# Performance work log

Measured on AMD Instinct MI355X. Metric: run time of the kernel, lower is better.

Reference implementation:

```python
import jax, jax.numpy as jnp
import numpy as np

# Module hyperparams (from init_kwargs)
MAX_DISP = 4
DILA = 1
P = 2 * MAX_DISP // DILA + 1  # patch_size = 9 -> 81 output channels


def setup_inputs() -> dict:
    key = jax.random.key(0)
    k0, k1 = jax.random.split(key)
    B, C, H, W = 4, 256, 96, 160
    return {
        "fmap0": jax.random.normal(k0, (B, C, H, W), dtype=jnp.float32),
        "fmap1": jax.random.normal(k1, (B, C, H, W), dtype=jnp.float32),
    }


def reference(fmap0, fmap1):
    """SpatialCorrelationSampler(kernel_size=1, patch_size=P, stride=1,
    padding=0, dilation=1, dilation_patch=DILA), reshaped to (B, P*P, H, W).

    corr[b, p, y, x] = sum_c fmap0[b,c,y,x] * fmap1[b,c,y+dy_p,x+dx_p]
    with (dy,dx) in {-MAX_DISP..MAX_DISP step DILA}; out-of-bounds -> 0
    (no channel normalization, matching the CUDA sampler).
    """
    B, C, H, W = fmap0.shape
    D = MAX_DISP
    # Zero-pad fmap1 so every displacement is a static-size slice.
    padded = jnp.pad(fmap1, ((0, 0), (0, 0), (D, D), (D, D)))
    oy, ox = jnp.meshgrid(jnp.arange(P) * DILA, jnp.arange(P) * DILA, indexing="ij")
    offs = jnp.stack([oy.ravel(), ox.ravel()], axis=1)  # (P*P, 2)

    def one_disp(off):
        # window of fmap1 shifted by (off - D): (B, C, H, W)
        win = jax.lax.dynamic_slice(padded, (0, 0, off[0], off[1]), (B, C, H, W))
        return jnp.einsum("bchw,bchw->bhw", fmap0, win)

    corr = jax.lax.map(one_disp, offs)  # (P*P, B, H, W), avoids P^2*C blowup
    return jnp.transpose(corr, (1, 0, 2, 3))  # (B, P*P, H, W)
```

## Files before the change

kernel.cpp:

```cpp
#include <hip/hip_runtime.h>


#define Bn 4
#define Cn 256
#define Hn 96
#define Wn 160
#define HWn (Hn * Wn)
#define NP 81
#define TY 16
#define TX 16
#define CCH 4
#define NSTAGE (Cn / CCH)
#define WROWS (TY + 8)
#define WCOLS (TX + 8)
#define SEGS (WCOLS / 4)
#define LROW 28
#define F1C (WROWS * LROW)
#define NT 576
#define F1CHUNK4 (CCH * HWn / 4)

__global__ __launch_bounds__(NT, 2) void corr_kernel(const float* __restrict__ f0,
                                                     const float* __restrict__ f1,
                                                     float* __restrict__ out) {
    __shared__ __align__(16) float lds[2 * CCH * F1C];

    const int tid  = threadIdx.x;
    const int wave = tid >> 6;
    const int lane = tid & 63;
    const int r    = lane >> 2;
    const int g    = lane & 3;

    const int tile = blockIdx.x;
    const int b    = tile / 60;
    const int rem  = tile % 60;
    const int ty   = rem / 10;
    const int tx   = rem - ty * 10;
    const int y0   = ty * TY;
    const int x0   = tx * TX;

    const int scc  = tid / (WROWS * SEGS);
    const int srm  = tid - scc * (WROWS * SEGS);
    const int srr  = srm / SEGS;
    const int sseg = srm - srr * SEGS;
    const int sgy  = y0 - 4 + srr;
    const int sgx  = x0 - 4 + sseg * 4;
    const bool sval = (sgy >= 0) && (sgy < Hn) && (sgx >= 0) && (sgx < Wn);
    const int slidx = (scc * F1C + srr * LROW + sseg * 4) >> 2;
    const int sgidx = sval ? ((((b * Cn + scc) * Hn + sgy) * Wn + sgx) >> 2) : 0;

    const float4* __restrict__ f1v = (const float4*)f1;
    float4* lv = (float4*)lds;

    float4 p1 = make_float4(0.f, 0.f, 0.f, 0.f);
    if (sval) p1 = f1v[sgidx];

    const float* f0s = f0 + ((b * Cn) * Hn + y0 + r) * Wn + x0 + g * 4;
    float4 p0[CCH];
#pragma unroll
    for (int cc = 0; cc < CCH; ++cc) p0[cc] = *(const float4*)(f0s + cc * HWn);

    float acc[9][4];
#pragma unroll
    for (int i = 0; i < 9; ++i)
#pragma unroll
        for (int j = 0; j < 4; ++j) acc[i][j] = 0.f;

    for (int s = 0; s < NSTAGE; ++s) {
        lv[(s & 1) * (CCH * F1C / 4) + slidx] = p1;
        __syncthreads();

        const int ns = (s + 1 < NSTAGE) ? s + 1 : NSTAGE - 1;
        float4 n1 = make_float4(0.f, 0.f, 0.f, 0.f);
        if (sval) n1 = f1v[sgidx + ns * F1CHUNK4];
        float4 n0[CCH];
#pragma unroll
        for (int cc = 0; cc < CCH; ++cc)
            n0[cc] = *(const float4*)(f0s + (ns * CCH + cc) * HWn);

        const float* base = &lds[(s & 1) * (CCH * F1C) + (r + wave) * LROW + g * 4];
#pragma unroll
        for (int cc = 0; cc < CCH; ++cc) {
            const float* wr = base + cc * F1C;
            float4 w0 = *(const float4*)(wr);
            float4 w1 = *(const float4*)(wr + 4);
            float4 w2 = *(const float4*)(wr + 8);
            float av[4]  = {p0[cc].x, p0[cc].y, p0[cc].z, p0[cc].w};
            float wv[12] = {w0.x, w0.y, w0.z, w0.w, w1.x, w1.y, w1.z, w1.w,
                            w2.x, w2.y, w2.z, w2.w};
#pragma unroll
            for (int dx = 0; dx < 9; ++dx)
#pragma unroll
                for (int rx = 0; rx < 4; ++rx)
                    acc[dx][rx] = fmaf(av[rx], wv[rx + dx], acc[dx][rx]);
        }

        p1 = n1;
#pragma unroll
        for (int cc = 0; cc < CCH; ++cc) p0[cc] = n0[cc];
    }

    const int orow = ((b * NP + wave * 9) * Hn + y0 + r) * Wn + x0 + g * 4;
#pragma unroll
    for (int dx = 0; dx < 9; ++dx)
        *(float4*)(out + orow + dx * HWn) =
            make_float4(acc[dx][0], acc[dx][1], acc[dx][2], acc[dx][3]);
}

extern "C" void kernel_launch(void* const* d_in, const int* in_sizes, int n_in,
                              void* d_out, int out_size, void* d_ws, size_t ws_size,
                              hipStream_t stream) {
    const float* f0 = (const float*)d_in[0];
    const float* f1 = (const float*)d_in[1];
    float* out = (float*)d_out;
    corr_kernel<<<dim3(240), NT, 0, stream>>>(f0, f1, out);
}
```

Baseline: 195.7 us.

## Double channels per pipeline stage and remap blocks for XCD-local L2 reuse

Each stage now covers 8 channels instead of 4, so the loop runs half as many iterations and half as many block barriers. Each thread stages two fmap1 float4s per stage, and each thread keeps 8 float4s of fmap0 current plus 8 prefetched. Block indices are also remapped so that blocks sharing the same XCD (blk&7) work on the same batch and neighbouring row tiles, with the aim of improving L2 locality for the overlapping halo. The main risk is register pressure: the doubled fmap0 buffers under launch_bounds(576,2) could cause spills or lower occupancy.

```diff
diff --git a/kernel.cpp b/kernel.cpp
--- a/kernel.cpp
+++ b/kernel.cpp
@@ -9,20 +9,20 @@
 #define NP 81
 #define TY 16
 #define TX 16
-#define CCH 4
+#define CCH 8
 #define NSTAGE (Cn / CCH)
 #define WROWS (TY + 8)
-#define WCOLS (TX + 8)
-#define SEGS (WCOLS / 4)
+#define SEGS 6
 #define LROW 28
 #define F1C (WROWS * LROW)
+#define BUF (CCH * F1C)
 #define NT 576
-#define F1CHUNK4 (CCH * HWn / 4)
+#define F1STG (CCH * HWn / 4)
 
 __global__ __launch_bounds__(NT, 2) void corr_kernel(const float* __restrict__ f0,
                                                      const float* __restrict__ f1,
                                                      float* __restrict__ out) {
-    __shared__ __align__(16) float lds[2 * CCH * F1C];
+    __shared__ __align__(16) float lds[2 * BUF];
 
     const int tid  = threadIdx.x;
     const int wave = tid >> 6;
@@ -30,13 +30,14 @@
     const int r    = lane >> 2;
     const int g    = lane & 3;
 
-    const int tile = blockIdx.x;
-    const int b    = tile / 60;
-    const int rem  = tile % 60;
-    const int ty   = rem / 10;
-    const int tx   = rem - ty * 10;
-    const int y0   = ty * TY;
-    const int x0   = tx * TX;
+    const int blk = blockIdx.x;
+    const int xcd = blk & 7;
+    const int it  = blk >> 3;
+    const int b   = xcd >> 1;
+    const int ty  = (xcd & 1) * 3 + it / 10;
+    const int tx  = it % 10;
+    const int y0  = ty * TY;
+    const int x0  = tx * TX;
 
     const int scc  = tid / (WROWS * SEGS);
     const int srm  = tid - scc * (WROWS * SEGS);
@@ -51,8 +52,8 @@
     const float4* __restrict__ f1v = (const float4*)f1;
     float4* lv = (float4*)lds;
 
-    float4 p1 = make_float4(0.f, 0.f, 0.f, 0.f);
-    if (sval) p1 = f1v[sgidx];
+    float4 p1a = make_float4(0.f, 0.f, 0.f, 0.f), p1b = p1a;
+    if (sval) { p1a = f1v[sgidx]; p1b = f1v[sgidx + HWn]; }
 
     const float* f0s = f0 + ((b * Cn) * Hn + y0 + r) * Wn + x0 + g * 4;
     float4 p0[CCH];
@@ -66,18 +67,20 @@
         for (int j = 0; j < 4; ++j) acc[i][j] = 0.f;
 
     for (int s = 0; s < NSTAGE; ++s) {
-        lv[(s & 1) * (CCH * F1C / 4) + slidx] = p1;
+        float4* buf = lv + (s & 1) * (BUF / 4);
+        buf[slidx]       = p1a;
+        buf[slidx + F1C] = p1b;
         __syncthreads();
 
         const int ns = (s + 1 < NSTAGE) ? s + 1 : NSTAGE - 1;
-        float4 n1 = make_float4(0.f, 0.f, 0.f, 0.f);
-        if (sval) n1 = f1v[sgidx + ns * F1CHUNK4];
+        float4 n1a = make_float4(0.f, 0.f, 0.f, 0.f), n1b = n1a;
+        if (sval) { n1a = f1v[sgidx + ns * F1STG]; n1b = f1v[sgidx + ns * F1STG + HWn]; }
         float4 n0[CCH];
 #pragma unroll
         for (int cc = 0; cc < CCH; ++cc)
             n0[cc] = *(const float4*)(f0s + (ns * CCH + cc) * HWn);
 
-        const float* base = &lds[(s & 1) * (CCH * F1C) + (r + wave) * LROW + g * 4];
+        const float* base = &lds[(s & 1) * BUF + (r + wave) * LROW + g * 4];
 #pragma unroll
         for (int cc = 0; cc < CCH; ++cc) {
             const float* wr = base + cc * F1C;
@@ -94,7 +97,7 @@
                     acc[dx][rx] = fmaf(av[rx], wv[rx + dx], acc[dx][rx]);
         }
 
-        p1 = n1;
+        p1a = n1a; p1b = n1b;
 #pragma unroll
         for (int cc = 0; cc < CCH; ++cc) p0[cc] = n0[cc];
     }
```

Result: faster. 182.8 us (-6.6%).
